# Optimization experiments

Measured on AMD Instinct MI355X. Metric: run time of the kernel, lower is better.

## Reference

```python
import jax, jax.numpy as jnp
import numpy as np

NB_HEAD = 16

def _rope_cos_sin(pos, dim):
    # Standard RoPE frequencies, base 10000, rotate-half convention.
    inv_freq = 1.0 / (10000.0 ** (jnp.arange(0, dim, 2, dtype=jnp.float32) / dim))  # (dim/2,)
    ang = pos.astype(jnp.float32)[:, None] * inv_freq[None, :]                      # (S, dim/2)
    ang = jnp.concatenate([ang, ang], axis=-1)                                      # (S, dim)
    return jnp.cos(ang), jnp.sin(ang)

def _rotate(x, cos, sin):
    # x: (B, H, S, hd); cos/sin: (S, hd) broadcast over B, H.
    h = x.shape[-1] // 2
    x1, x2 = x[..., :h], x[..., h:]
    return x * cos + jnp.concatenate([-x2, x1], axis=-1) * sin

def setup_inputs() -> dict:
    key = jax.random.key(0)
    ks = jax.random.split(key, 8)
    B, S, D = 2, 2048, 1024
    scale = 0.02
    return {
        'query': jax.random.normal(ks[0], (B, S, D), dtype=jnp.float32),
        'key':   jax.random.normal(ks[1], (B, S, D), dtype=jnp.float32),
        'value': jax.random.normal(ks[2], (B, S, D), dtype=jnp.float32),
        'pos_enc': jnp.arange(S, dtype=jnp.int32),
        'Wk': jax.random.normal(ks[3], (D, D), dtype=jnp.float32) * scale,
        'bk': jnp.zeros((D,), dtype=jnp.float32),
        'Wv': jax.random.normal(ks[4], (D, D), dtype=jnp.float32) * scale,
        'bv': jnp.zeros((D,), dtype=jnp.float32),
        'Wo': jax.random.normal(ks[5], (D, D), dtype=jnp.float32) * scale,
        'bo': jnp.zeros((D,), dtype=jnp.float32),
    }

def reference(query, key, value, pos_enc, Wk, bk, Wv, bv, Wo, bo):
    B, S, D = query.shape
    H = NB_HEAD
    hd = D // H
    # Faithful quirk: raw reshape (B,S,D)->(B,H,S,hd), NO transpose; query unprojected.
    q = query.reshape(B, H, S, hd)
    k = (key @ Wk.T + bk).reshape(B, H, S, hd)
    v = (value @ Wv.T + bv).reshape(B, H, S, hd)
    cos, sin = _rope_cos_sin(pos_enc, hd)
    q = _rotate(q, cos, sin)
    k = _rotate(k, cos, sin)
    v = _rotate(v, cos, sin)  # RoPE applied to V as well (faithful)
    scores = jnp.einsum('bhqd,bhkd->bhqk', q, k) / jnp.sqrt(jnp.float32(hd))
    # tril(-1) + triu(1): zero the diagonal (NOT -inf masking)
    scores = scores * (1.0 - jnp.eye(S, dtype=scores.dtype))
    # softmax over dim=2 == the QUERY axis (faithful quirk)
    attn = jax.nn.softmax(scores, axis=2)
    out = jnp.einsum('bhqk,bhkd->bhqd', attn, v)     # (B,H,S,hd)
    x = out.transpose(0, 2, 1, 3).reshape(B, S, D)   # (B,S,D)
    return x @ Wo.T + bo
```

## Files before the change

kernel.cpp:

```cpp
#include <hip/hip_runtime.h>
#include <hip/hip_bf16.h>
#include <math.h>

#define B_  2
#define S_  2048
#define D_  1024
#define H_  16
#define HD_ 64
#define M_  (B_*S_)
#define BH_ (B_*H_)
#define QKSCALE 0.18033688011112042f

typedef __attribute__((ext_vector_type(8)))  short  bf16x8;
typedef __attribute__((ext_vector_type(4)))  float  f32x4;

#define MFMA16(a,b,c) __builtin_amdgcn_mfma_f32_16x16x32_bf16(a,b,c,0,0,0)

__device__ float          g_vp[(size_t)M_ * D_];
__device__ float          g_p1[(size_t)M_ * D_];
__device__ float          g_p2[(size_t)M_ * D_];
__device__ float          g_p3[(size_t)M_ * D_];
__device__ unsigned short g_q16[(size_t)M_ * D_];
__device__ unsigned short g_k16[(size_t)M_ * D_];
__device__ unsigned short g_v16t[(size_t)M_ * D_];
__device__ unsigned short g_x16[(size_t)M_ * D_];
__device__ float          g_rz[BH_ * S_];
__device__ float          g_tab[S_ * 64];

static __device__ __forceinline__ unsigned short f2b(float x){
  union { float f; unsigned u; } v; v.f = x;
  unsigned r = v.u + 0x7FFFu + ((v.u >> 16) & 1u);
  return (unsigned short)(r >> 16);
}
static __device__ __forceinline__ unsigned cvtpk(float lo, float hi){
  unsigned r;
  asm("v_cvt_pk_bf16_f32 %0, %1, %2" : "=v"(r) : "v"(lo), "v"(hi));
  return r;
}

__global__ void k_table(const int* __restrict__ pos){
  int i = blockIdx.x * 256 + threadIdx.x;
  if (i >= S_ * 32) return;
  int s = i >> 5, f = i & 31;
  float ang = (float)pos[s] * powf(10000.0f, -(float)f * (1.0f/32.0f));
  g_tab[2*i]   = cosf(ang);
  g_tab[2*i+1] = sinf(ang);
}

__global__ void k_ropeq(const float* __restrict__ in){
  const int i = blockIdx.x * 256 + threadIdx.x;
  const int grp = i >> 5, d = i & 31;
  const int s = grp & (S_ - 1);
  const size_t base = (size_t)grp * 64;
  const float x1 = in[base + d];
  const float x2 = in[base + d + 32];
  const float c  = g_tab[(s*32 + d)*2];
  const float sn = g_tab[(s*32 + d)*2 + 1];
  g_q16[base + d]      = f2b((x1*c - x2*sn) * QKSCALE);
  g_q16[base + d + 32] = f2b((x2*c + x1*sn) * QKSCALE);
}

__global__ __launch_bounds__(256) void k_proj(const float* __restrict__ key,
                                              const float* __restrict__ value,
                                              const float* __restrict__ Wk,
                                              const float* __restrict__ bk,
                                              const float* __restrict__ Wv,
                                              const float* __restrict__ bv){
  __shared__ __align__(16) unsigned short As[128*64];
  __shared__ __align__(16) unsigned short Bs[128*64];
  const int z = blockIdx.z;
  const float* A    = z ? value : key;
  const float* W    = z ? Wv : Wk;
  const float* bias = z ? bv : bk;
  const int t = threadIdx.x, l = t & 63, wid = t >> 6;
  const int wm = wid >> 1, wn = wid & 1;
  const int rowB = blockIdx.y * 128, colB = blockIdx.x * 128;
  f32x4 acc[4][4];
  #pragma unroll
  for (int i = 0; i < 4; ++i)
    #pragma unroll
    for (int j = 0; j < 4; ++j)
      #pragma unroll
      for (int r = 0; r < 4; ++r) acc[i][j][r] = 0.f;

  const int srow = t >> 3, se = (t & 7) * 8;
  float4 a0[4], a1[4], b0[4], b1[4];
#define GLD(K0) \
  for (int u = 0; u < 4; ++u){ \
    const int row = srow + u*32; \
    const float* ap = A + (size_t)(rowB+row)*D_ + (K0) + se; \
    const float* wp = W + (size_t)(colB+row)*D_ + (K0) + se; \
    a0[u] = *(const float4*)ap; a1[u] = *(const float4*)(ap+4); \
    b0[u] = *(const float4*)wp; b1[u] = *(const float4*)(wp+4); \
  }
  GLD(0);
  for (int k0 = 0; k0 < D_; k0 += 64){
    __syncthreads();
    #pragma unroll
    for (int u = 0; u < 4; ++u){
      const int row = srow + u*32;
      const int off = row*128 + ((se*2) ^ ((row & 7) << 4));
      uint4 pa, pb;
      pa.x = cvtpk(a0[u].x, a0[u].y); pa.y = cvtpk(a0[u].z, a0[u].w);
      pa.z = cvtpk(a1[u].x, a1[u].y); pa.w = cvtpk(a1[u].z, a1[u].w);
      pb.x = cvtpk(b0[u].x, b0[u].y); pb.y = cvtpk(b0[u].z, b0[u].w);
      pb.z = cvtpk(b1[u].x, b1[u].y); pb.w = cvtpk(b1[u].z, b1[u].w);
      *(uint4*)((char*)As + off) = pa;
      *(uint4*)((char*)Bs + off) = pb;
    }
    __syncthreads();
    if (k0 + 64 < D_){ GLD(k0 + 64); }
    #pragma unroll
    for (int kk = 0; kk < 2; ++kk){
      const int cb = kk*64 + (l >> 4) * 16;
      bf16x8 af[4], bfr[4];
      #pragma unroll
      for (int mi = 0; mi < 4; ++mi){
        const int row = wm*64 + mi*16 + (l & 15);
        af[mi] = *(const bf16x8*)((const char*)As + row*128 + (cb ^ ((row & 7) << 4)));
      }
      #pragma unroll
      for (int ni = 0; ni < 4; ++ni){
        const int row = wn*64 + ni*16 + (l & 15);
        bfr[ni] = *(const bf16x8*)((const char*)Bs + row*128 + (cb ^ ((row & 7) << 4)));
      }
      #pragma unroll
      for (int mi = 0; mi < 4; ++mi)
        #pragma unroll
        for (int ni = 0; ni < 4; ++ni)
          acc[mi][ni] = MFMA16(af[mi], bfr[ni], acc[mi][ni]);
    }
  }
#undef GLD
  const int ql15 = l & 15, r4 = (l >> 4) * 4;
  const int hcol = (colB >> 6) + wn;
  #pragma unroll
  for (int mi = 0; mi < 4; ++mi){
    #pragma unroll
    for (int r = 0; r < 4; ++r){
      const int row = rowB + wm*64 + mi*16 + r4 + r;
      const int pos = ((row & 127) << 4) + hcol;
      #pragma unroll
      for (int ni = 0; ni < 2; ++ni){
        const int col = colB + wn*64 + ni*16 + ql15;
        const int f = ni*16 + ql15;
        const float c  = g_tab[(pos*32 + f)*2];
        const float sn = g_tab[(pos*32 + f)*2 + 1];
        const float x1 = acc[mi][ni][r]   + bias[col];
        const float x2 = acc[mi][ni+2][r] + bias[col+32];
        const float o1 = x1*c - x2*sn;
        const float o2 = x2*c + x1*sn;
        if (z){
          g_vp[(size_t)row*D_ + col]      = o1;
          g_vp[(size_t)row*D_ + col + 32] = o2;
        } else {
          g_k16[(size_t)row*D_ + col]      = f2b(o1);
          g_k16[(size_t)row*D_ + col + 32] = f2b(o2);
        }
      }
    }
  }
}

__global__ __launch_bounds__(256) void k_gemm_out(const unsigned short* __restrict__ A,
                                                  const float* __restrict__ W,
                                                  const float* __restrict__ bias,
                                                  float* __restrict__ C){
  __shared__ __align__(16) unsigned short As[128*64];
  __shared__ __align__(16) unsigned short Bs[128*64];
  const int t = threadIdx.x, l = t & 63, wid = t >> 6;
  const int wm = wid >> 1, wn = wid & 1;
  const int rowB = blockIdx.y * 128, colB = blockIdx.x * 128;
  f32x4 acc[4][4];
  #pragma unroll
  for (int i = 0; i < 4; ++i)
    #pragma unroll
    for (int j = 0; j < 4; ++j)
      #pragma unroll
      for (int r = 0; r < 4; ++r) acc[i][j][r] = 0.f;

  const int srow = t >> 3, se = (t & 7) * 8, scb = (t & 7) * 16;
  float4 ar[4], b0[4], b1[4];
#define GLD(K0) \
  for (int u = 0; u < 4; ++u){ \
    const int row = srow + u*32; \
    ar[u] = *(const float4*)((const char*)(A + (size_t)(rowB+row)*D_ + (K0)) + scb); \
    const float* wp = W + (size_t)(colB+row)*D_ + (K0) + se; \
    b0[u] = *(const float4*)wp; b1[u] = *(const float4*)(wp+4); \
  }
  GLD(0);
  for (int k0 = 0; k0 < D_; k0 += 64){
    __syncthreads();
    #pragma unroll
    for (int u = 0; u < 4; ++u){
      const int row = srow + u*32;
      const int off = row*128 + (scb ^ ((row & 7) << 4));
      uint4 pb;
      pb.x = cvtpk(b0[u].x, b0[u].y); pb.y = cvtpk(b0[u].z, b0[u].w);
      pb.z = cvtpk(b1[u].x, b1[u].y); pb.w = cvtpk(b1[u].z, b1[u].w);
      *(float4*)((char*)As + off) = ar[u];
      *(uint4*)((char*)Bs + off) = pb;
    }
    __syncthreads();
    if (k0 + 64 < D_){ GLD(k0 + 64); }
    #pragma unroll
    for (int kk = 0; kk < 2; ++kk){
      const int cb = kk*64 + (l >> 4) * 16;
      bf16x8 af[4], bfr[4];
      #pragma unroll
      for (int mi = 0; mi < 4; ++mi){
        const int row = wm*64 + mi*16 + (l & 15);
        af[mi] = *(const bf16x8*)((const char*)As + row*128 + (cb ^ ((row & 7) << 4)));
      }
      #pragma unroll
      for (int ni = 0; ni < 4; ++ni){
        const int row = wn*64 + ni*16 + (l & 15);
        bfr[ni] = *(const bf16x8*)((const char*)Bs + row*128 + (cb ^ ((row & 7) << 4)));
      }
      #pragma unroll
      for (int mi = 0; mi < 4; ++mi)
        #pragma unroll
        for (int ni = 0; ni < 4; ++ni)
          acc[mi][ni] = MFMA16(af[mi], bfr[ni], acc[mi][ni]);
    }
  }
#undef GLD
  #pragma unroll
  for (int mi = 0; mi < 4; ++mi){
    #pragma unroll
    for (int ni = 0; ni < 4; ++ni){
      const int col = colB + wn*64 + ni*16 + (l & 15);
      const float bb = bias[col];
      #pragma unroll
      for (int r = 0; r < 4; ++r){
        const int row = rowB + wm*64 + mi*16 + (l >> 4)*4 + r;
        C[(size_t)row * D_ + col] = acc[mi][ni][r] + bb;
      }
    }
  }
}

__global__ __launch_bounds__(256) void k_pass1(){
  __shared__ float zs[4][4][16];
  const int t = threadIdx.x, l = t & 63, wid = t >> 6;
  const int bh = blockIdx.y;
  const int kwb = blockIdx.x * 64;
  const unsigned short* Qp = g_q16 + (size_t)bh * S_ * HD_;
  const unsigned short* Kp = g_k16 + (size_t)bh * S_ * HD_;
  bf16x8 bk_[4][2];
  #pragma unroll
  for (int kb = 0; kb < 4; ++kb){
    const unsigned short* kr = Kp + (size_t)(kwb + kb*16 + (l & 15)) * HD_ + (l >> 4) * 8;
    bk_[kb][0] = *(const bf16x8*)(kr);
    bk_[kb][1] = *(const bf16x8*)(kr + 32);
  }
  float zz[4] = {0.f, 0.f, 0.f, 0.f};
  const int qBeg = wid * (S_/4);
  for (int qi = 0; qi < S_/4; qi += 16){
    const int q0 = qBeg + qi;
    const unsigned short* qr = Qp + (size_t)(q0 + (l & 15)) * HD_ + (l >> 4) * 8;
    bf16x8 a0 = *(const bf16x8*)(qr);
    bf16x8 a1 = *(const bf16x8*)(qr + 32);
    #pragma unroll
    for (int kb = 0; kb < 4; ++kb){
      f32x4 c = {0.f, 0.f, 0.f, 0.f};
      c = MFMA16(a0, bk_[kb][0], c);
      c = MFMA16(a1, bk_[kb][1], c);
      if (q0 == kwb + kb*16){
        const int kg = kwb + kb*16 + (l & 15);
        #pragma unroll
        for (int r = 0; r < 4; ++r)
          zz[kb] += (q0 + (l >> 4)*4 + r == kg) ? 1.0f : exp2f(c[r]);
      } else {
        zz[kb] += exp2f(c[0]) + exp2f(c[1]) + exp2f(c[2]) + exp2f(c[3]);
      }
    }
  }
  #pragma unroll
  for (int kb = 0; kb < 4; ++kb){
    float z = zz[kb];
    z += __shfl_xor(z, 16); z += __shfl_xor(z, 32);
    if (l < 16) zs[wid][kb][l] = z;
  }
  __syncthreads();
  if (t < 64){
    const int kb = t >> 4, ki = t & 15;
    const float Z = zs[0][kb][ki] + zs[1][kb][ki] + zs[2][kb][ki] + zs[3][kb][ki];
    g_rz[bh*S_ + kwb + kb*16 + ki] = 1.0f / Z;
  }
}

__global__ __launch_bounds__(256) void k_vfix(){
  __shared__ __align__(16) float tile[64][68];
  const int t = threadIdx.x;
  const int bh = blockIdx.y;
  const int s0 = blockIdx.x * 64;
  #pragma unroll
  for (int u = 0; u < 4; ++u){
    const int i = t + u*256;
    const int row = i >> 4, c4 = (i & 15) * 4;
    *(float4*)&tile[row][c4] = *(const float4*)(g_vp + (size_t)(bh*S_ + s0 + row) * HD_ + c4);
  }
  __syncthreads();
  const int d = t >> 2;
  const int sc = (t & 3) * 16;
  float rzv[16];
  #pragma unroll
  for (int u = 0; u < 4; ++u)
    *(float4*)&rzv[u*4] = *(const float4*)(g_rz + bh*S_ + s0 + sc + u*4);
  unsigned w[8];
  #pragma unroll
  for (int j2 = 0; j2 < 8; ++j2)
    w[j2] = cvtpk(tile[sc + 2*j2][d] * rzv[2*j2], tile[sc + 2*j2 + 1][d] * rzv[2*j2 + 1]);
  unsigned short* dst = g_v16t + (size_t)(bh*HD_ + d) * S_ + s0 + sc;
  *(uint4*)(dst)     = *(uint4*)&w[0];
  *(uint4*)(dst + 8) = *(uint4*)&w[4];
}

__global__ __launch_bounds__(256, 4) void k_pass2(){
  __shared__ __align__(16) unsigned short Ks[2][64*64];
  __shared__ __align__(16) unsigned short Vs[2][64*64];
  const int t = threadIdx.x, l = t & 63, wid = t >> 6;
  const int bh = blockIdx.y;
  const int z = blockIdx.z;
  const int b = bh >> 4, hh = bh & 15;
  const int q0 = blockIdx.x * 128;
  const unsigned short* Qp = g_q16  + (size_t)bh * S_ * HD_;
  const unsigned short* Kp = g_k16  + (size_t)bh * S_ * HD_;
  const unsigned short* Vp = g_v16t + (size_t)bh * HD_ * S_;
  float* Op = (z == 0) ? g_vp : (z == 1) ? g_p1 : (z == 2) ? g_p2 : g_p3;
  const int ql = l & 15, kq = l >> 4;
  const int qb = q0 + wid*32;

  bf16x8 qf[2][2];
  #pragma unroll
  for (int h = 0; h < 2; ++h){
    const unsigned short* qr = Qp + (size_t)(qb + h*16 + ql) * HD_ + kq * 8;
    qf[h][0] = *(const bf16x8*)(qr);
    qf[h][1] = *(const bf16x8*)(qr + 32);
  }
  f32x4 co[4][2];
  #pragma unroll
  for (int nd = 0; nd < 4; ++nd)
    #pragma unroll
    for (int h = 0; h < 2; ++h)
      #pragma unroll
      for (int r = 0; r < 4; ++r) co[nd][h][r] = 0.f;

  const int srow = t >> 3, j = t & 7;
  const int scb = j * 16;
  const int vsl = j >> 2, jp = j & 3;
  const int kg0 = z * (S_/4);
  float4 kreg[2];
  uint2 vA[2], vB[2];

#define LOADREGS(KT) \
  { const int kk0 = kg0 + (KT)*64; \
    _Pragma("unroll") \
    for (int u = 0; u < 2; ++u){ \
      const int row = srow + u*32; \
      kreg[u] = *(const float4*)((const char*)(Kp + (size_t)(kk0 + row) * HD_) + scb); \
      const unsigned short* vb = Vp + (size_t)row * S_ + kk0 + vsl*32 + jp*4; \
      vA[u] = *(const uint2*)(vb); \
      vB[u] = *(const uint2*)(vb + 16); \
    } }
#define WRITEBUF(BUF) \
  { _Pragma("unroll") \
    for (int u = 0; u < 2; ++u){ \
      const int row = srow + u*32; \
      const int off = row*128 + (scb ^ ((row & 7) << 4)); \
      *(float4*)((char*)Ks[BUF] + off) = kreg[u]; \
      uint4 wv; wv.x = vA[u].x; wv.y = vA[u].y; wv.z = vB[u].x; wv.w = vB[u].y; \
      *(uint4*)((char*)Vs[BUF] + off) = wv; \
    } }

  LOADREGS(0);
  WRITEBUF(0);
  LOADREGS(1);
  __syncthreads();

  for (int kt = 0; kt < 8; ++kt){
    const int k0 = kg0 + kt * 64;
    const int cur = kt & 1;
    if (kt < 7){ WRITEBUF(cur ^ 1); }
    if (kt < 6){ LOADREGS(kt + 2); }
    f32x4 cst[4][2];
    #pragma unroll
    for (int kb = 0; kb < 4; ++kb)
      #pragma unroll
      for (int h = 0; h < 2; ++h)
        #pragma unroll
        for (int r = 0; r < 4; ++r) cst[kb][h][r] = 0.f;
    #pragma unroll
    for (int kb = 0; kb < 4; ++kb){
      const int row = kb*16 + ql;
      #pragma unroll
      for (int s = 0; s < 2; ++s){
        bf16x8 kf = *(const bf16x8*)((const char*)Ks[cur] + row*128 + ((s*64 + kq*16) ^ ((row & 7) << 4)));
        cst[kb][0] = MFMA16(kf, qf[0][s], cst[kb][0]);
        cst[kb][1] = MFMA16(kf, qf[1][s], cst[kb][1]);
      }
    }
    const bool diag = (k0 < qb + 32) && (qb < k0 + 64);
    uint2 Pr[2][4];
    #pragma unroll
    for (int h = 0; h < 2; ++h){
      const int qg = qb + h*16 + ql;
      #pragma unroll
      for (int kb = 0; kb < 4; ++kb){
        float e[4];
        if (diag){
          #pragma unroll
          for (int r = 0; r < 4; ++r){
            const int key = k0 + kb*16 + kq*4 + r;
            e[r] = (qg == key) ? 1.0f : exp2f(cst[kb][h][r]);
          }
        } else {
          #pragma unroll
          for (int r = 0; r < 4; ++r) e[r] = exp2f(cst[kb][h][r]);
        }
        Pr[h][kb].x = cvtpk(e[0], e[1]);
        Pr[h][kb].y = cvtpk(e[2], e[3]);
      }
    }
    #pragma unroll
    for (int g = 0; g < 2; ++g){
      union { unsigned u[4]; bf16x8 v; } ap0, ap1;
      ap0.u[0] = Pr[0][2*g].x;   ap0.u[1] = Pr[0][2*g].y;
      ap0.u[2] = Pr[0][2*g+1].x; ap0.u[3] = Pr[0][2*g+1].y;
      ap1.u[0] = Pr[1][2*g].x;   ap1.u[1] = Pr[1][2*g].y;
      ap1.u[2] = Pr[1][2*g+1].x; ap1.u[3] = Pr[1][2*g+1].y;
      #pragma unroll
      for (int nd = 0; nd < 4; ++nd){
        const int row = nd*16 + ql;
        bf16x8 vf = *(const bf16x8*)((const char*)Vs[cur] + row*128 + ((g*64 + kq*16) ^ ((row & 7) << 4)));
        co[nd][0] = MFMA16(ap0.v, vf, co[nd][0]);
        co[nd][1] = MFMA16(ap1.v, vf, co[nd][1]);
      }
    }
    __syncthreads();
  }
#undef LOADREGS
#undef WRITEBUF
  #pragma unroll
  for (int h = 0; h < 2; ++h){
    #pragma unroll
    for (int nd = 0; nd < 4; ++nd){
      const int d = nd*16 + ql;
      #pragma unroll
      for (int r = 0; r < 4; ++r){
        const int q = qb + h*16 + kq*4 + r;
        Op[(size_t)(b*S_ + q) * D_ + hh*HD_ + d] = co[nd][h][r];
      }
    }
  }
}

__global__ void k_reduce(){
  const int i = blockIdx.x * 256 + threadIdx.x;
  const size_t off = (size_t)i * 8;
  float4 a0 = *(const float4*)(g_vp + off), a1 = *(const float4*)(g_vp + off + 4);
  float4 b0 = *(const float4*)(g_p1 + off), b1 = *(const float4*)(g_p1 + off + 4);
  float4 c0 = *(const float4*)(g_p2 + off), c1 = *(const float4*)(g_p2 + off + 4);
  float4 d0 = *(const float4*)(g_p3 + off), d1 = *(const float4*)(g_p3 + off + 4);
  uint4 w;
  w.x = cvtpk(a0.x + b0.x + c0.x + d0.x, a0.y + b0.y + c0.y + d0.y);
  w.y = cvtpk(a0.z + b0.z + c0.z + d0.z, a0.w + b0.w + c0.w + d0.w);
  w.z = cvtpk(a1.x + b1.x + c1.x + d1.x, a1.y + b1.y + c1.y + d1.y);
  w.w = cvtpk(a1.z + b1.z + c1.z + d1.z, a1.w + b1.w + c1.w + d1.w);
  *(uint4*)(g_x16 + off) = w;
}

extern "C" void kernel_launch(void* const* d_in, const int* in_sizes, int n_in,
                              void* d_out, int out_size, void* d_ws, size_t ws_size,
                              hipStream_t stream) {
  const float* query = (const float*)d_in[0];
  const float* key   = (const float*)d_in[1];
  const float* value = (const float*)d_in[2];
  const int*   pos   = (const int*)  d_in[3];
  const float* Wk    = (const float*)d_in[4];
  const float* bk    = (const float*)d_in[5];
  const float* Wv    = (const float*)d_in[6];
  const float* bv    = (const float*)d_in[7];
  const float* Wo    = (const float*)d_in[8];
  const float* bo    = (const float*)d_in[9];
  float* out = (float*)d_out;

  unsigned short* px16; hipGetSymbolAddress((void**)&px16, HIP_SYMBOL(g_x16));

  k_table<<<256, 256, 0, stream>>>(pos);

  dim3 gP(D_/128, M_/128, 2);
  k_proj<<<gP, 256, 0, stream>>>(key, value, Wk, bk, Wv, bv);

  k_ropeq<<<8192, 256, 0, stream>>>(query);

  k_pass1<<<dim3(S_/64, BH_), 256, 0, stream>>>();
  k_vfix <<<dim3(32, BH_), 256, 0, stream>>>();
  k_pass2<<<dim3(16, BH_, 4), 256, 0, stream>>>();
  k_reduce<<<(M_*D_/8)/256, 256, 0, stream>>>();

  dim3 gO(D_/128, M_/128);
  k_gemm_out<<<gO, 256, 0, stream>>>(px16, Wo, bo, out);
}
```

Measured before the change: 233.4 us.

## Pre-convert GEMM operands to bf16 and double-buffer with direct global-to-LDS loads

A new kernel converts key, value, Wk, Wv and Wo from fp32 to bf16 up front. The projection and output GEMMs then load bf16 tiles straight into double-buffered shared memory with global_load_lds, replacing the register-staged fp32 load, convert and store path. This removes in-loop conversion work and one barrier per k-step, and lets the next tile load overlap the MFMA work. In exchange it adds an extra pass over the inputs (read fp32, write bf16), doubles LDS use, and relies on global_load_lds and the XOR swizzle producing the correct layout.

```diff
diff --git a/kernel.cpp b/kernel.cpp
--- a/kernel.cpp
+++ b/kernel.cpp
@@ -20,6 +20,11 @@
 __device__ float          g_p1[(size_t)M_ * D_];
 __device__ float          g_p2[(size_t)M_ * D_];
 __device__ float          g_p3[(size_t)M_ * D_];
+__device__ unsigned short g_key16[(size_t)M_ * D_];
+__device__ unsigned short g_val16[(size_t)M_ * D_];
+__device__ unsigned short g_wk16[(size_t)D_ * D_];
+__device__ unsigned short g_wv16[(size_t)D_ * D_];
+__device__ unsigned short g_wo16[(size_t)D_ * D_];
 __device__ unsigned short g_q16[(size_t)M_ * D_];
 __device__ unsigned short g_k16[(size_t)M_ * D_];
 __device__ unsigned short g_v16t[(size_t)M_ * D_];
@@ -36,6 +41,10 @@
   unsigned r;
   asm("v_cvt_pk_bf16_f32 %0, %1, %2" : "=v"(r) : "v"(lo), "v"(hi));
   return r;
+}
+static __device__ __forceinline__ void gld16(const void* g, void* l){
+  __builtin_amdgcn_global_load_lds((const __attribute__((address_space(1))) void*)g,
+                                   (__attribute__((address_space(3))) void*)l, 16, 0, 0);
 }
 
 __global__ void k_table(const int* __restrict__ pos){
@@ -45,6 +54,23 @@
   float ang = (float)pos[s] * powf(10000.0f, -(float)f * (1.0f/32.0f));
   g_tab[2*i]   = cosf(ang);
   g_tab[2*i+1] = sinf(ang);
+}
+
+__global__ void k_cvt5(const float* __restrict__ key, const float* __restrict__ value,
+                       const float* __restrict__ Wk, const float* __restrict__ Wv,
+                       const float* __restrict__ Wo){
+  const int z = blockIdx.z;
+  const float* src = (z==0)?key:(z==1)?value:(z==2)?Wk:(z==3)?Wv:Wo;
+  unsigned short* dst = (z==0)?g_key16:(z==1)?g_val16:(z==2)?g_wk16:(z==3)?g_wv16:g_wo16;
+  const int n8 = (z < 2) ? (M_*D_/8) : (D_*D_/8);
+  const int i = blockIdx.x * 256 + threadIdx.x;
+  if (i >= n8) return;
+  float4 a = *(const float4*)(src + (size_t)i*8);
+  float4 b = *(const float4*)(src + (size_t)i*8 + 4);
+  uint4 w;
+  w.x = cvtpk(a.x, a.y); w.y = cvtpk(a.z, a.w);
+  w.z = cvtpk(b.x, b.y); w.w = cvtpk(b.z, b.w);
+  *(uint4*)(dst + (size_t)i*8) = w;
 }
 
 __global__ void k_ropeq(const float* __restrict__ in){
@@ -60,17 +86,13 @@
   g_q16[base + d + 32] = f2b((x2*c + x1*sn) * QKSCALE);
 }
 
-__global__ __launch_bounds__(256) void k_proj(const float* __restrict__ key,
-                                              const float* __restrict__ value,
-                                              const float* __restrict__ Wk,
-                                              const float* __restrict__ bk,
-                                              const float* __restrict__ Wv,
+__global__ __launch_bounds__(256) void k_proj(const float* __restrict__ bk,
                                               const float* __restrict__ bv){
-  __shared__ __align__(16) unsigned short As[128*64];
-  __shared__ __align__(16) unsigned short Bs[128*64];
+  __shared__ __align__(16) unsigned short As[2][128*64];
+  __shared__ __align__(16) unsigned short Bs[2][128*64];
   const int z = blockIdx.z;
-  const float* A    = z ? value : key;
-  const float* W    = z ? Wv : Wk;
+  const unsigned short* A = z ? g_val16 : g_key16;
+  const unsigned short* W = z ? g_wv16  : g_wk16;
   const float* bias = z ? bv : bk;
   const int t = threadIdx.x, l = t & 63, wid = t >> 6;
   const int wm = wid >> 1, wn = wid & 1;
@@ -83,33 +105,23 @@
       #pragma unroll
       for (int r = 0; r < 4; ++r) acc[i][j][r] = 0.f;
 
-  const int srow = t >> 3, se = (t & 7) * 8;
-  float4 a0[4], a1[4], b0[4], b1[4];
-#define GLD(K0) \
-  for (int u = 0; u < 4; ++u){ \
-    const int row = srow + u*32; \
-    const float* ap = A + (size_t)(rowB+row)*D_ + (K0) + se; \
-    const float* wp = W + (size_t)(colB+row)*D_ + (K0) + se; \
-    a0[u] = *(const float4*)ap; a1[u] = *(const float4*)(ap+4); \
-    b0[u] = *(const float4*)wp; b1[u] = *(const float4*)(wp+4); \
-  }
-  GLD(0);
-  for (int k0 = 0; k0 < D_; k0 += 64){
+  const int lrow = l >> 3;
+  const int scol = ((l & 7) << 4) ^ (lrow << 4);
+
+#define ISSUE(BUF, K0) \
+  { _Pragma("unroll") \
+    for (int ii = 0; ii < 4; ++ii){ \
+      const int c = wid*4 + ii; \
+      const int row = c*8 + lrow; \
+      gld16((const char*)(A + (size_t)(rowB + row)*D_ + (K0)) + scol, (char*)As[BUF] + c*1024); \
+      gld16((const char*)(W + (size_t)(colB + row)*D_ + (K0)) + scol, (char*)Bs[BUF] + c*1024); \
+    } }
+
+  ISSUE(0, 0);
+  for (int kt = 0; kt < 16; ++kt){
+    const int cur = kt & 1;
     __syncthreads();
-    #pragma unroll
-    for (int u = 0; u < 4; ++u){
-      const int row = srow + u*32;
-      const int off = row*128 + ((se*2) ^ ((row & 7) << 4));
-      uint4 pa, pb;
-      pa.x = cvtpk(a0[u].x, a0[u].y); pa.y = cvtpk(a0[u].z, a0[u].w);
-      pa.z = cvtpk(a1[u].x, a1[u].y); pa.w = cvtpk(a1[u].z, a1[u].w);
-      pb.x = cvtpk(b0[u].x, b0[u].y); pb.y = cvtpk(b0[u].z, b0[u].w);
-      pb.z = cvtpk(b1[u].x, b1[u].y); pb.w = cvtpk(b1[u].z, b1[u].w);
-      *(uint4*)((char*)As + off) = pa;
-      *(uint4*)((char*)Bs + off) = pb;
-    }
-    __syncthreads();
-    if (k0 + 64 < D_){ GLD(k0 + 64); }
+    if (kt < 15){ ISSUE(cur ^ 1, (kt+1)*64); }
     #pragma unroll
     for (int kk = 0; kk < 2; ++kk){
       const int cb = kk*64 + (l >> 4) * 16;
@@ -117,12 +129,12 @@
       #pragma unroll
       for (int mi = 0; mi < 4; ++mi){
         const int row = wm*64 + mi*16 + (l & 15);
-        af[mi] = *(const bf16x8*)((const char*)As + row*128 + (cb ^ ((row & 7) << 4)));
+        af[mi] = *(const bf16x8*)((const char*)As[cur] + row*128 + (cb ^ ((row & 7) << 4)));
       }
       #pragma unroll
       for (int ni = 0; ni < 4; ++ni){
         const int row = wn*64 + ni*16 + (l & 15);
-        bfr[ni] = *(const bf16x8*)((const char*)Bs + row*128 + (cb ^ ((row & 7) << 4)));
+        bfr[ni] = *(const bf16x8*)((const char*)Bs[cur] + row*128 + (cb ^ ((row & 7) << 4)));
       }
       #pragma unroll
       for (int mi = 0; mi < 4; ++mi)
@@ -131,7 +143,7 @@
           acc[mi][ni] = MFMA16(af[mi], bfr[ni], acc[mi][ni]);
     }
   }
-#undef GLD
+#undef ISSUE
   const int ql15 = l & 15, r4 = (l >> 4) * 4;
   const int hcol = (colB >> 6) + wn;
   #pragma unroll
@@ -162,12 +174,12 @@
   }
 }
 
-__global__ __launch_bounds__(256) void k_gemm_out(const unsigned short* __restrict__ A,
-                                                  const float* __restrict__ W,
-                                                  const float* __restrict__ bias,
+__global__ __launch_bounds__(256) void k_gemm_out(const float* __restrict__ bias,
                                                   float* __restrict__ C){
-  __shared__ __align__(16) unsigned short As[128*64];
-  __shared__ __align__(16) unsigned short Bs[128*64];
+  __shared__ __align__(16) unsigned short As[2][128*64];
+  __shared__ __align__(16) unsigned short Bs[2][128*64];
+  const unsigned short* A = g_x16;
+  const unsigned short* W = g_wo16;
   const int t = threadIdx.x, l = t & 63, wid = t >> 6;
   const int wm = wid >> 1, wn = wid & 1;
   const int rowB = blockIdx.y * 128, colB = blockIdx.x * 128;
@@ -179,30 +191,23 @@
       #pragma unroll
       for (int r = 0; r < 4; ++r) acc[i][j][r] = 0.f;
 
-  const int srow = t >> 3, se = (t & 7) * 8, scb = (t & 7) * 16;
-  float4 ar[4], b0[4], b1[4];
-#define GLD(K0) \
-  for (int u = 0; u < 4; ++u){ \
-    const int row = srow + u*32; \
-    ar[u] = *(const float4*)((const char*)(A + (size_t)(rowB+row)*D_ + (K0)) + scb); \
-    const float* wp = W + (size_t)(colB+row)*D_ + (K0) + se; \
-    b0[u] = *(const float4*)wp; b1[u] = *(const float4*)(wp+4); \
-  }
-  GLD(0);
-  for (int k0 = 0; k0 < D_; k0 += 64){
+  const int lrow = l >> 3;
+  const int scol = ((l & 7) << 4) ^ (lrow << 4);
+
+#define ISSUE(BUF, K0) \
+  { _Pragma("unroll") \
+    for (int ii = 0; ii < 4; ++ii){ \
+      const int c = wid*4 + ii; \
+      const int row = c*8 + lrow; \
+      gld16((const char*)(A + (size_t)(rowB + row)*D_ + (K0)) + scol, (char*)As[BUF] + c*1024); \
+      gld16((const char*)(W + (size_t)(colB + row)*D_ + (K0)) + scol, (char*)Bs[BUF] + c*1024); \
+    } }
+
+  ISSUE(0, 0);
+  for (int kt = 0; kt < 16; ++kt){
+    const int cur = kt & 1;
     __syncthreads();
-    #pragma unroll
-    for (int u = 0; u < 4; ++u){
-      const int row = srow + u*32;
-      const int off = row*128 + (scb ^ ((row & 7) << 4));
-      uint4 pb;
-      pb.x = cvtpk(b0[u].x, b0[u].y); pb.y = cvtpk(b0[u].z, b0[u].w);
-      pb.z = cvtpk(b1[u].x, b1[u].y); pb.w = cvtpk(b1[u].z, b1[u].w);
-      *(float4*)((char*)As + off) = ar[u];
-      *(uint4*)((char*)Bs + off) = pb;
-    }
-    __syncthreads();
-    if (k0 + 64 < D_){ GLD(k0 + 64); }
+    if (kt < 15){ ISSUE(cur ^ 1, (kt+1)*64); }
     #pragma unroll
     for (int kk = 0; kk < 2; ++kk){
       const int cb = kk*64 + (l >> 4) * 16;
@@ -210,12 +215,12 @@
       #pragma unroll
       for (int mi = 0; mi < 4; ++mi){
         const int row = wm*64 + mi*16 + (l & 15);
-        af[mi] = *(const bf16x8*)((const char*)As + row*128 + (cb ^ ((row & 7) << 4)));
+        af[mi] = *(const bf16x8*)((const char*)As[cur] + row*128 + (cb ^ ((row & 7) << 4)));
       }
       #pragma unroll
       for (int ni = 0; ni < 4; ++ni){
         const int row = wn*64 + ni*16 + (l & 15);
-        bfr[ni] = *(const bf16x8*)((const char*)Bs + row*128 + (cb ^ ((row & 7) << 4)));
+        bfr[ni] = *(const bf16x8*)((const char*)Bs[cur] + row*128 + (cb ^ ((row & 7) << 4)));
       }
       #pragma unroll
       for (int mi = 0; mi < 4; ++mi)
@@ -224,7 +229,7 @@
           acc[mi][ni] = MFMA16(af[mi], bfr[ni], acc[mi][ni]);
     }
   }
-#undef GLD
+#undef ISSUE
   #pragma unroll
   for (int mi = 0; mi < 4; ++mi){
     #pragma unroll
@@ -486,12 +491,11 @@
   const float* bo    = (const float*)d_in[9];
   float* out = (float*)d_out;
 
-  unsigned short* px16; hipGetSymbolAddress((void**)&px16, HIP_SYMBOL(g_x16));
-
   k_table<<<256, 256, 0, stream>>>(pos);
+  k_cvt5<<<dim3(2048, 1, 5), 256, 0, stream>>>(key, value, Wk, Wv, Wo);
 
   dim3 gP(D_/128, M_/128, 2);
-  k_proj<<<gP, 256, 0, stream>>>(key, value, Wk, bk, Wv, bv);
+  k_proj<<<gP, 256, 0, stream>>>(bk, bv);
 
   k_ropeq<<<8192, 256, 0, stream>>>(query);
 
@@ -501,5 +505,5 @@
   k_reduce<<<(M_*D_/8)/256, 256, 0, stream>>>();
 
   dim3 gO(D_/128, M_/128);
-  k_gemm_out<<<gO, 256, 0, stream>>>(px16, Wo, bo, out);
-}
+  k_gemm_out<<<gO, 256, 0, stream>>>(bo, out);
+}
```

Result: faster. 225.8 us (-3.2%).
